# Optimization experiments

Measured on AMD Instinct MI355X. Metric: run time of the kernel, lower is better.

Reference implementation:

```python
import math
import jax, jax.numpy as jnp
import numpy as np

B, T = 4, 512
STATE_DIM, ACT_DIM = 17, 18
H, NH, L, MAXT = 1024, 16, 4, 4096
S = 3 * T          # interleaved (rtg, state, action) sequence length
D = H // NH
FF = 4 * H
LN_EPS = 1e-5


def setup_inputs() -> dict:
    key = jax.random.key(0)
    ks = jax.random.split(key, 32)
    init = lambda k, shape: jax.random.normal(k, shape, jnp.float32) * 0.02
    inp = {
        "states": jax.random.normal(ks[0], (B, T, STATE_DIM), jnp.float32),
        "returns_to_go": jax.random.normal(ks[1], (B, T, 1), jnp.float32),
        "timesteps": jax.random.randint(ks[2], (B, T), 0, MAXT),
        "actions": jax.random.randint(ks[3], (B, T), 0, ACT_DIM),
        "bandera": 0,
        # embeddings / input projections
        "embed_time_table": init(ks[4], (MAXT, H)),
        "embed_act_table": init(ks[5], (ACT_DIM, H)),
        "Wrtg": init(ks[6], (1, H)), "brtg": jnp.zeros((H,), jnp.float32),
        "Wst": init(ks[7], (STATE_DIM, H)), "bst": jnp.zeros((H,), jnp.float32),
        # per-block params, stacked over L layers
        "Wq": init(ks[8], (L, H, H)), "bq": jnp.zeros((L, H), jnp.float32),
        "Wk": init(ks[9], (L, H, H)), "bk": jnp.zeros((L, H), jnp.float32),
        "Wv": init(ks[10], (L, H, H)), "bv": jnp.zeros((L, H), jnp.float32),
        "Wo": init(ks[11], (L, H, H)), "bo": jnp.zeros((L, H), jnp.float32),
        "W1": init(ks[12], (L, H, FF)), "b1": jnp.zeros((L, FF), jnp.float32),
        "W2": init(ks[13], (L, FF, H)), "b2": jnp.zeros((L, H), jnp.float32),
        # prediction heads
        "Wpr": init(ks[14], (H, 1)), "bpr": jnp.zeros((1,), jnp.float32),
        "Wps": init(ks[15], (H, STATE_DIM)), "bps": jnp.zeros((STATE_DIM,), jnp.float32),
        "Wpa": init(ks[16], (H, ACT_DIM)), "bpa": jnp.zeros((ACT_DIM,), jnp.float32),
    }
    return inp


def _ln(x):
    # LayerNorm, elementwise_affine=False
    m = jnp.mean(x, axis=-1, keepdims=True)
    v = jnp.mean((x - m) ** 2, axis=-1, keepdims=True)
    return (x - m) * jax.lax.rsqrt(v + LN_EPS)


def reference(states, returns_to_go, embed_time_table, embed_act_table,
              Wrtg, brtg, Wst, bst,
              Wq, bq, Wk, bk, Wv, bv, Wo, bo,
              W1, b1, W2, b2,
              Wpr, bpr, Wps, bps, Wpa, bpa,
              timesteps, actions, bandera):
    te = embed_time_table[timesteps]                      # [B,T,H]
    r = returns_to_go @ Wrtg + brtg + te                  # [B,T,H]
    s = states @ Wst + bst + te                           # [B,T,H]
    a = embed_act_table[actions] + te                     # [B,T,H]
    # interleave (r_t, s_t, a_t) along time -> [B, 3T, H]
    h = jnp.stack([r, s, a], axis=2).reshape(B, S, H)
    h = _ln(h)
    mask = jnp.tril(jnp.ones((S, S), bool))
    scale = 1.0 / math.sqrt(D)
    for i in range(L):
        q = (h @ Wq[i] + bq[i]).reshape(B, S, NH, D).transpose(0, 2, 1, 3)
        k = (h @ Wk[i] + bk[i]).reshape(B, S, NH, D).transpose(0, 2, 1, 3)
        v = (h @ Wv[i] + bv[i]).reshape(B, S, NH, D).transpose(0, 2, 1, 3)
        sc = jnp.einsum('bhqd,bhkd->bhqk', q, k) * scale  # [B,NH,S,S]
        sc = jnp.where(mask, sc, -jnp.inf)
        att = jax.nn.softmax(sc, axis=-1)
        o = jnp.einsum('bhqk,bhkd->bhqd', att, v)
        o = o.transpose(0, 2, 1, 3).reshape(B, S, H)
        h = _ln(h + o @ Wo[i] + bo[i])
        m = jax.nn.gelu(h @ W1[i] + b1[i], approximate=False) @ W2[i] + b2[i]
        h = _ln(h + m)
    hh = h.reshape(B, T, 3, H)
    h_s = hh[:, :, 1]   # token after (..., r_t, s_t)
    h_a = hh[:, :, 2]   # token after (..., r_t, s_t, a_t)
    return_preds = h_a @ Wpr + bpr                        # [B,T,1]
    state_preds = h_a @ Wps + bps                         # [B,T,STATE_DIM]
    action_preds = h_s @ Wpa + bpa                        # [B,T,ACT_DIM]
    return (state_preds, action_preds, return_preds)
```

## Files before the change

### kernel.cpp

```cpp
#include <hip/hip_runtime.h>
#include <hip/hip_bf16.h>
#include <math.h>

#define Bc 4
#define Tc 512
#define Sc 1536
#define Hc 1024
#define NHc 16
#define Dc 64
#define FFc 4096
#define Lc 4
#define Mrows (Bc*Tc*3)
#define LN_EPS 1e-5f

typedef __attribute__((ext_vector_type(4))) float  f32x4;
typedef __attribute__((ext_vector_type(8))) short  s16x8;
typedef __attribute__((ext_vector_type(4))) short  s16x4;

__device__ __forceinline__ short f2b(float f) {
    union { __hip_bfloat16 h; short s; } u;
    u.h = __float2bfloat16(f);
    return u.s;
}

__device__ __forceinline__ void gload16(const void* g, void* l) {
    __builtin_amdgcn_global_load_lds(
        (const __attribute__((address_space(1))) void*)g,
        (__attribute__((address_space(3))) void*)l, 16, 0, 0);
}

__global__ __launch_bounds__(256) void embed_kernel(
    const float* __restrict__ states, const float* __restrict__ rtg,
    const int* __restrict__ timesteps, const int* __restrict__ actions,
    const float* __restrict__ ett, const float* __restrict__ eat,
    const float* __restrict__ Wrtg, const float* __restrict__ brtg,
    const float* __restrict__ Wst, const float* __restrict__ bst,
    float* __restrict__ h)
{
    const int bt = blockIdx.x;
    const int b = bt / Tc, t = bt % Tc;
    const int ts = timesteps[bt];
    const int ac = actions[bt];
    const float rv = rtg[bt];
    const float* te = ett + (size_t)ts * Hc;
    const float* ea = eat + (size_t)ac * Hc;
    __shared__ float sst[17];
    if (threadIdx.x < 17) sst[threadIdx.x] = states[bt * 17 + threadIdx.x];
    __syncthreads();
    float* hr = h + ((size_t)b * Sc + 3 * t) * Hc;
    for (int j = threadIdx.x; j < Hc; j += 256) {
        const float tej = te[j];
        hr[j] = rv * Wrtg[j] + brtg[j] + tej;
        float sv = bst[j];
        #pragma unroll
        for (int qx = 0; qx < 17; ++qx) sv += sst[qx] * Wst[qx * Hc + j];
        hr[Hc + j] = sv + tej;
        hr[2 * Hc + j] = ea[j] + tej;
    }
}

__global__ __launch_bounds__(256) void resln_kernel(float* __restrict__ h,
                                                    const float* __restrict__ add,
                                                    short* __restrict__ hb)
{
    const size_t row = blockIdx.x;
    float4* hr = reinterpret_cast<float4*>(h + row * Hc);
    const int tid = threadIdx.x;
    float4 x = hr[tid];
    if (add != nullptr) {
        const float4 a = reinterpret_cast<const float4*>(add + row * Hc)[tid];
        x.x += a.x; x.y += a.y; x.z += a.z; x.w += a.w;
    }
    float s1 = x.x + x.y + x.z + x.w;
    float s2 = x.x*x.x + x.y*x.y + x.z*x.z + x.w*x.w;
    #pragma unroll
    for (int off = 32; off > 0; off >>= 1) {
        s1 += __shfl_xor(s1, off);
        s2 += __shfl_xor(s2, off);
    }
    __shared__ float r1[4], r2[4];
    const int wv = tid >> 6, lane = tid & 63;
    if (lane == 0) { r1[wv] = s1; r2[wv] = s2; }
    __syncthreads();
    s1 = r1[0] + r1[1] + r1[2] + r1[3];
    s2 = r2[0] + r2[1] + r2[2] + r2[3];
    const float mean = s1 * (1.0f / Hc);
    const float var  = s2 * (1.0f / Hc) - mean * mean;
    const float rs = rsqrtf(var + LN_EPS);
    x.x = (x.x - mean) * rs; x.y = (x.y - mean) * rs;
    x.z = (x.z - mean) * rs; x.w = (x.w - mean) * rs;
    hr[tid] = x;
    if (hb != nullptr) {
        s16x4 o; o[0] = f2b(x.x); o[1] = f2b(x.y); o[2] = f2b(x.z); o[3] = f2b(x.w);
        *(s16x4*)&hb[row * Hc + tid * 4] = o;
    }
}

__global__ __launch_bounds__(256) void wconv_all_kernel(
    const float* __restrict__ Wq, const float* __restrict__ Wk,
    const float* __restrict__ Wv, const float* __restrict__ Wo,
    const float* __restrict__ W1, const float* __restrict__ W2,
    short* __restrict__ wqkv_t, short* __restrict__ wo_t,
    short* __restrict__ w1_t, short* __restrict__ w2_t)
{
    __shared__ float Ls[64][68];
    const int blk = blockIdx.x;
    const float* src; short* dst; int N, dstStride, dstRow0, tx, ty;
    if (blk < 1024) {
        const int m = blk >> 8;
        const int local = blk & 255;
        tx = local & 15; ty = local >> 4;
        N = 1024; dstStride = 1024;
        if (m == 0)      { src = Wq; dst = wqkv_t; dstRow0 = 0; }
        else if (m == 1) { src = Wk; dst = wqkv_t; dstRow0 = 1024; }
        else if (m == 2) { src = Wv; dst = wqkv_t; dstRow0 = 2048; }
        else             { src = Wo; dst = wo_t;   dstRow0 = 0; }
    } else if (blk < 2048) {
        const int local = blk - 1024;
        tx = local & 63; ty = local >> 6;
        src = W1; dst = w1_t; N = 4096; dstStride = 1024; dstRow0 = 0;
    } else {
        const int local = blk - 2048;
        tx = local & 15; ty = local >> 4;
        src = W2; dst = w2_t; N = 1024; dstStride = 4096; dstRow0 = 0;
    }
    const int n0 = tx * 64, k0 = ty * 64;
    const int tid = threadIdx.x;
    #pragma unroll
    for (int it = 0; it < 4; ++it) {
        const int idx = tid + 256 * it;
        const int r = idx >> 4, c4 = idx & 15;
        *(f32x4*)&Ls[r][c4 * 4] = *(const f32x4*)(src + (size_t)(k0 + r) * N + n0 + c4 * 4);
    }
    __syncthreads();
    #pragma unroll
    for (int it = 0; it < 2; ++it) {
        const int idx = tid + 256 * it;
        const int n = idx & 63, k8 = idx >> 6;
        s16x8 o;
        #pragma unroll
        for (int j = 0; j < 8; ++j) o[j] = f2b(Ls[k8 * 8 + j][n]);
        *(s16x8*)(dst + (size_t)(dstRow0 + n0 + n) * dstStride + k0 + k8 * 8) = o;
    }
}

__global__ __launch_bounds__(256) void biaspack_kernel(
    const float* __restrict__ bq, const float* __restrict__ bk,
    const float* __restrict__ bv, float* __restrict__ pb)
{
    const int idx = blockIdx.x * 256 + threadIdx.x;
    const int l = idx / 3072, j = idx % 3072;
    float v;
    if (j < 1024) v = bq[l * 1024 + j];
    else if (j < 2048) v = bk[l * 1024 + j - 1024];
    else v = bv[l * 1024 + j - 2048];
    pb[idx] = v;
}

__global__ __launch_bounds__(256) void headspack_kernel(
    const float* __restrict__ Wps, const float* __restrict__ bps,
    const float* __restrict__ Wpr, const float* __restrict__ bpr,
    const float* __restrict__ Wpa, const float* __restrict__ bpa,
    short* __restrict__ Wha, short* __restrict__ Whb,
    float* __restrict__ biasA, float* __restrict__ biasB)
{
    const int n = blockIdx.x & 63, set = blockIdx.x >> 6;
    const int tid = threadIdx.x;
    if (tid == 0) {
        if (set == 0) biasA[n] = (n < 17) ? bps[n] : (n == 17 ? bpr[0] : 0.f);
        else          biasB[n] = (n < 18) ? bpa[n] : 0.f;
    }
    short* dst = (set == 0 ? Wha : Whb) + (size_t)n * 1024;
    for (int k = tid; k < 1024; k += 256) {
        float v;
        if (set == 0) v = (n < 17) ? Wps[(size_t)k * 17 + n] : (n == 17 ? Wpr[k] : 0.f);
        else          v = (n < 18) ? Wpa[(size_t)k * 18 + n] : 0.f;
        dst[k] = f2b(v);
    }
}

__global__ __launch_bounds__(256) void headsgather_kernel(
    const float* __restrict__ scrA, const float* __restrict__ scrB,
    float* __restrict__ out)
{
    const int idx = blockIdx.x * 256 + threadIdx.x;
    if (idx >= 2048 * 36) return;
    const int bt = idx / 36, j = idx % 36;
    if (j < 17)      out[bt * 17 + j] = scrA[bt * 64 + j];
    else if (j < 35) out[2048 * 17 + bt * 18 + (j - 17)] = scrB[bt * 64 + (j - 17)];
    else             out[2048 * 35 + bt] = scrA[bt * 64 + 17];
}

template<int BN, int DO_GELU, int OUTBF16>
__global__ __launch_bounds__(256) void gemm_bb(
    const short* __restrict__ A, const short* __restrict__ Bt,
    const float* __restrict__ bias, void* __restrict__ Cv,
    int M, int N, int K, int arm, int aro)
{
    constexpr int NJ = BN / 32;
    __shared__ short As[2 * 128 * 32];
    __shared__ short Bs[2 * BN * 32];
    const int tid = threadIdx.x, lane = tid & 63, wid = tid >> 6;
    const int wr = wid >> 1, wc = wid & 1;
    const int g = lane >> 4, ql = lane & 15;
    const int m0 = blockIdx.y * 128, n0 = blockIdx.x * BN;

    const int crow = lane >> 2;
    const int ccol = (lane & 3) * 8;

    const short* Ag0 = A + ((size_t)arm * (m0 + wid * 32 + crow) + aro) * K + ccol;
    const short* Ag1 = A + ((size_t)arm * (m0 + wid * 32 + 16 + crow) + aro) * K + ccol;
    const int a0off = (wid * 32) * 32;
    const int a1off = (wid * 32 + 16) * 32;

    const short* Bg0; const short* Bg1 = nullptr;
    int b0off = 0, b1off = 0;
    if constexpr (BN == 128) {
        Bg0 = Bt + (size_t)(n0 + wid * 32 + crow) * K + ccol;
        Bg1 = Bt + (size_t)(n0 + wid * 32 + 16 + crow) * K + ccol;
        b0off = (wid * 32) * 32;
        b1off = (wid * 32 + 16) * 32;
    } else {
        Bg0 = Bt + (size_t)(n0 + wid * 16 + crow) * K + ccol;
        b0off = (wid * 16) * 32;
    }

    auto stage = [&](int buf, int k0) {
        short* Ab = &As[buf * (128 * 32)];
        short* Bb = &Bs[buf * (BN * 32)];
        gload16(Ag0 + k0, Ab + a0off);
        gload16(Ag1 + k0, Ab + a1off);
        gload16(Bg0 + k0, Bb + b0off);
        if constexpr (BN == 128) gload16(Bg1 + k0, Bb + b1off);
    };

    f32x4 acc[4][NJ] = {};
    stage(0, 0);
    int cur = 0;
    for (int k0 = 0; k0 < K; k0 += 32) {
        __syncthreads();
        if (k0 + 32 < K) stage(cur ^ 1, k0 + 32);
        const short* Acur = &As[cur * (128 * 32)];
        const short* Bcur = &Bs[cur * (BN * 32)];
        s16x8 af[4], bfr[NJ];
        #pragma unroll
        for (int mi = 0; mi < 4; ++mi)
            af[mi] = *(const s16x8*)&Acur[(wr * 64 + mi * 16 + ql) * 32 + g * 8];
        #pragma unroll
        for (int nj = 0; nj < NJ; ++nj)
            bfr[nj] = *(const s16x8*)&Bcur[(wc * (BN / 2) + nj * 16 + ql) * 32 + g * 8];
        #pragma unroll
        for (int mi = 0; mi < 4; ++mi)
            #pragma unroll
            for (int nj = 0; nj < NJ; ++nj)
                acc[mi][nj] = __builtin_amdgcn_mfma_f32_16x16x32_bf16(
                    af[mi], bfr[nj], acc[mi][nj], 0, 0, 0);
        cur ^= 1;
    }

    #pragma unroll
    for (int mi = 0; mi < 4; ++mi) {
        #pragma unroll
        for (int nj = 0; nj < NJ; ++nj) {
            const int col = n0 + wc * (BN / 2) + nj * 16 + ql;
            const float bv = bias[col];
            #pragma unroll
            for (int r = 0; r < 4; ++r) {
                const int row = m0 + wr * 64 + mi * 16 + g * 4 + r;
                float v = acc[mi][nj][r] + bv;
                if constexpr (DO_GELU)
                    v = 0.5f * v * (1.0f + erff(v * 0.70710678118654752f));
                if constexpr (OUTBF16)
                    ((short*)Cv)[(size_t)row * N + col] = f2b(v);
                else
                    ((float*)Cv)[(size_t)row * N + col] = v;
            }
        }
    }
}

template<int BN, int ABF16, int DO_GELU, int OUTBF16>
__global__ __launch_bounds__(256) void gemm_mfma(
    const void* __restrict__ Av, const float* __restrict__ Wg,
    const float* __restrict__ bias, void* __restrict__ Cv,
    int M, int N, int K, int ldw)
{
    constexpr int NJ = BN / 32;
    __shared__ short As[128][32];
    __shared__ short Bs[BN][40];
    const int tid  = threadIdx.x;
    const int lane = tid & 63;
    const int wid  = tid >> 6;
    const int wr   = wid >> 1, wc = wid & 1;
    const int m0 = blockIdx.y * 128;
    const int n0 = blockIdx.x * BN;

    const int  wn4  = tid >> 3;
    const int  wk4  = (tid & 7) * 4;
    const bool wact = tid < 2 * BN;

    f32x4 areg[4]; s16x8 abreg[2]; f32x4 wreg[4];

    auto loadA = [&](int k0) {
        if constexpr (!ABF16) {
            const float* A = (const float*)Av;
            #pragma unroll
            for (int i = 0; i < 4; ++i) {
                const int idx = tid + 256 * i;
                const int r = idx >> 3, c4 = idx & 7;
                areg[i] = *(const f32x4*)(A + (size_t)(m0 + r) * K + k0 + c4 * 4);
            }
        } else {
            const short* A = (const short*)Av;
            #pragma unroll
            for (int i = 0; i < 2; ++i) {
                const int idx = tid + 256 * i;
                const int r = idx >> 2, c = idx & 3;
                abreg[i] = *(const s16x8*)(A + (size_t)(m0 + r) * K + k0 + c * 8);
            }
        }
    };
    auto loadW = [&](int k0) {
        if (wact) {
            #pragma unroll
            for (int i = 0; i < 4; ++i)
                wreg[i] = *(const f32x4*)(Wg + (size_t)(k0 + wk4 + i) * ldw + n0 + wn4 * 4);
        }
    };
    auto stage = [&]() {
        if constexpr (!ABF16) {
            #pragma unroll
            for (int i = 0; i < 4; ++i) {
                const int idx = tid + 256 * i;
                const int r = idx >> 3, c4 = idx & 7;
                s16x4 s;
                #pragma unroll
                for (int j = 0; j < 4; ++j) s[j] = f2b(areg[i][j]);
                *(s16x4*)&As[r][c4 * 4] = s;
            }
        } else {
            #pragma unroll
            for (int i = 0; i < 2; ++i) {
                const int idx = tid + 256 * i;
                const int r = idx >> 2, c = idx & 3;
                *(s16x8*)&As[r][c * 8] = abreg[i];
            }
        }
        if (wact) {
            #pragma unroll
            for (int j = 0; j < 4; ++j) {
                s16x4 o;
                #pragma unroll
                for (int i = 0; i < 4; ++i) o[i] = f2b(wreg[i][j]);
                *(s16x4*)&Bs[wn4 * 4 + j][wk4] = o;
            }
        }
    };

    f32x4 acc[4][NJ] = {};

    loadA(0); loadW(0);
    for (int k0 = 0; k0 < K; k0 += 32) {
        __syncthreads();
        stage();
        __syncthreads();
        if (k0 + 32 < K) { loadA(k0 + 32); loadW(k0 + 32); }
        s16x8 af[4], bfr[NJ];
        #pragma unroll
        for (int mi = 0; mi < 4; ++mi)
            af[mi] = *(const s16x8*)&As[wr * 64 + mi * 16 + (lane & 15)][(lane >> 4) * 8];
        #pragma unroll
        for (int nj = 0; nj < NJ; ++nj)
            bfr[nj] = *(const s16x8*)&Bs[wc * (BN / 2) + nj * 16 + (lane & 15)][(lane >> 4) * 8];
        #pragma unroll
        for (int mi = 0; mi < 4; ++mi)
            #pragma unroll
            for (int nj = 0; nj < NJ; ++nj)
                acc[mi][nj] = __builtin_amdgcn_mfma_f32_16x16x32_bf16(
                    af[mi], bfr[nj], acc[mi][nj], 0, 0, 0);
    }

    #pragma unroll
    for (int mi = 0; mi < 4; ++mi) {
        #pragma unroll
        for (int nj = 0; nj < NJ; ++nj) {
            const int col = n0 + wc * (BN / 2) + nj * 16 + (lane & 15);
            const float bv = bias[col];
            #pragma unroll
            for (int r = 0; r < 4; ++r) {
                const int row = m0 + wr * 64 + mi * 16 + (lane >> 4) * 4 + r;
                float v = acc[mi][nj][r] + bv;
                if constexpr (DO_GELU)
                    v = 0.5f * v * (1.0f + erff(v * 0.70710678118654752f));
                if constexpr (OUTBF16)
                    ((short*)Cv)[(size_t)row * N + col] = f2b(v);
                else
                    ((float*)Cv)[(size_t)row * N + col] = v;
            }
        }
    }
}

__global__ __launch_bounds__(256) void vtrans_kernel(
    const short* __restrict__ v, int vs, short* __restrict__ vt)
{
    const int nkt = Sc / 64;
    const int blk = blockIdx.x;
    const int bh = blk / nkt, kt = blk % nkt;
    const int b = bh / NHc, hh = bh % NHc;
    __shared__ short Ls[64][64];
    const int tid = threadIdx.x;
    #pragma unroll
    for (int i = 0; i < 2; ++i) {
        const int idx = tid + 256 * i;
        const int r = idx >> 3, c8 = idx & 7;
        const int cs = c8 ^ (r & 7) ^ (r >> 3);
        *(s16x8*)&Ls[r][cs * 8] =
            *(const s16x8*)(v + ((size_t)(b * Sc + kt * 64 + r)) * vs + hh * 64 + c8 * 8);
    }
    __syncthreads();
    #pragma unroll
    for (int i = 0; i < 2; ++i) {
        const int idx = tid + 256 * i;
        const int d = idx >> 3, k8 = idx & 7;
        s16x8 o;
        #pragma unroll
        for (int j = 0; j < 8; ++j) {
            const int kv = k8 * 8 + j;
            const int cs = (d >> 3) ^ (kv & 7) ^ (kv >> 3);
            o[j] = Ls[kv][cs * 8 + (d & 7)];
        }
        *(s16x8*)(vt + ((size_t)bh * 64 + d) * Sc + kt * 64 + k8 * 8) = o;
    }
}

__global__ __launch_bounds__(256) void attn_kernel(
    const short* __restrict__ qg, const short* __restrict__ kg,
    const short* __restrict__ vtg, short* __restrict__ og, int qks)
{
    const int nqt = Sc / 64;
    const int blk = blockIdx.x;
    const int bh = blk / nqt;
    const int qt = (nqt - 1) - (blk % nqt);
    const int b = bh / NHc, hh = bh % NHc;
    const int tid = threadIdx.x, lane = tid & 63, w = tid >> 6;
    const int g = lane >> 4, ql = lane & 15;

    __shared__ short Qs[64][72];
    __shared__ short Ks[64][72];
    __shared__ short Vs[64][72];
    __shared__ short Ps[4][16][72];

    const size_t baseq = ((size_t)b * Sc) * qks + hh * Dc;

    #pragma unroll
    for (int i = 0; i < 2; ++i) {
        const int idx = tid + 256 * i;
        const int r = idx >> 3, c8 = idx & 7;
        *(s16x8*)&Qs[r][c8 * 8] =
            *(const s16x8*)(qg + baseq + (size_t)(qt * 64 + r) * qks + c8 * 8);
    }
    __syncthreads();
    const s16x8 bq0 = *(const s16x8*)&Qs[w * 16 + ql][g * 8];
    const s16x8 bq1 = *(const s16x8*)&Qs[w * 16 + ql][32 + g * 8];

    f32x4 acc_o[4] = {};
    float m = -1e30f, l = 0.f;
    const int qrow = qt * 64 + w * 16 + ql;

    for (int kt = 0; kt <= qt; ++kt) {
        __syncthreads();
        #pragma unroll
        for (int i = 0; i < 2; ++i) {
            const int idx = tid + 256 * i;
            const int r = idx >> 3, c8 = idx & 7;
            *(s16x8*)&Ks[r][c8 * 8] =
                *(const s16x8*)(kg + baseq + (size_t)(kt * 64 + r) * qks + c8 * 8);
            *(s16x8*)&Vs[r][c8 * 8] =
                *(const s16x8*)(vtg + ((size_t)bh * 64 + r) * Sc + kt * 64 + c8 * 8);
        }
        __syncthreads();

        f32x4 sacc[4] = {};
        #pragma unroll
        for (int mi = 0; mi < 4; ++mi) {
            const s16x8 a0 = *(const s16x8*)&Ks[mi * 16 + ql][g * 8];
            const s16x8 a1 = *(const s16x8*)&Ks[mi * 16 + ql][32 + g * 8];
            sacc[mi] = __builtin_amdgcn_mfma_f32_16x16x32_bf16(a0, bq0, sacc[mi], 0, 0, 0);
            sacc[mi] = __builtin_amdgcn_mfma_f32_16x16x32_bf16(a1, bq1, sacc[mi], 0, 0, 0);
        }

        float pv[16];
        float pm = -1e30f;
        #pragma unroll
        for (int mi = 0; mi < 4; ++mi)
            #pragma unroll
            for (int r = 0; r < 4; ++r) {
                const int kv = kt * 64 + mi * 16 + g * 4 + r;
                const float s = (kv <= qrow) ? sacc[mi][r] * 0.125f : -1e30f;
                pv[mi * 4 + r] = s;
                pm = fmaxf(pm, s);
            }
        pm = fmaxf(pm, __shfl_xor(pm, 16));
        pm = fmaxf(pm, __shfl_xor(pm, 32));
        const float m2 = fmaxf(m, pm);
        const float corr = __expf(m - m2);
        m = m2;
        float ps = 0.f;
        #pragma unroll
        for (int i = 0; i < 16; ++i) { pv[i] = __expf(pv[i] - m2); ps += pv[i]; }
        ps += __shfl_xor(ps, 16);
        ps += __shfl_xor(ps, 32);
        l = l * corr + ps;

        #pragma unroll
        for (int mi = 0; mi < 4; ++mi) {
            s16x4 pw;
            #pragma unroll
            for (int r = 0; r < 4; ++r) pw[r] = f2b(pv[mi * 4 + r]);
            *(s16x4*)&Ps[w][ql][mi * 16 + g * 4] = pw;
        }

        float corr_r[4];
        #pragma unroll
        for (int r = 0; r < 4; ++r) corr_r[r] = __shfl(corr, g * 4 + r);
        #pragma unroll
        for (int nj = 0; nj < 4; ++nj)
            #pragma unroll
            for (int r = 0; r < 4; ++r) acc_o[nj][r] *= corr_r[r];

        const s16x8 pa0 = *(const s16x8*)&Ps[w][ql][g * 8];
        const s16x8 pa1 = *(const s16x8*)&Ps[w][ql][32 + g * 8];
        #pragma unroll
        for (int nj = 0; nj < 4; ++nj) {
            const s16x8 v0 = *(const s16x8*)&Vs[nj * 16 + ql][g * 8];
            const s16x8 v1 = *(const s16x8*)&Vs[nj * 16 + ql][32 + g * 8];
            acc_o[nj] = __builtin_amdgcn_mfma_f32_16x16x32_bf16(pa0, v0, acc_o[nj], 0, 0, 0);
            acc_o[nj] = __builtin_amdgcn_mfma_f32_16x16x32_bf16(pa1, v1, acc_o[nj], 0, 0, 0);
        }
    }

    const float rl = 1.0f / l;
    float rl_r[4];
    #pragma unroll
    for (int r = 0; r < 4; ++r) rl_r[r] = __shfl(rl, g * 4 + r);
    const size_t baseo = ((size_t)b * Sc) * Hc + hh * Dc;
    #pragma unroll
    for (int nj = 0; nj < 4; ++nj)
        #pragma unroll
        for (int r = 0; r < 4; ++r) {
            const int qr = qt * 64 + w * 16 + g * 4 + r;
            og[baseo + (size_t)qr * Hc + nj * 16 + ql] = f2b(acc_o[nj][r] * rl_r[r]);
        }
}

__global__ __launch_bounds__(64) void heads_kernel(
    const float* __restrict__ h,
    const float* __restrict__ Wpr, const float* __restrict__ bpr,
    const float* __restrict__ Wps, const float* __restrict__ bps,
    const float* __restrict__ Wpa, const float* __restrict__ bpa,
    float* __restrict__ out)
{
    const int bt = blockIdx.x;
    const int b = bt / Tc, t = bt % Tc;
    const float* hs = h + ((size_t)b * Sc + 3 * t + 1) * Hc;
    const float* ha = h + ((size_t)b * Sc + 3 * t + 2) * Hc;
    __shared__ float shs[Hc], sha[Hc];
    for (int i = threadIdx.x; i < Hc; i += 64) { shs[i] = hs[i]; sha[i] = ha[i]; }
    __syncthreads();
    const int j = threadIdx.x;
    if (j < 17) {
        float a = bps[j];
        for (int kx = 0; kx < Hc; ++kx) a += sha[kx] * Wps[kx * 17 + j];
        out[bt * 17 + j] = a;
    } else if (j < 35) {
        const int jj = j - 17;
        float a = bpa[jj];
        for (int kx = 0; kx < Hc; ++kx) a += shs[kx] * Wpa[kx * 18 + jj];
        out[Bc * Tc * 17 + bt * 18 + jj] = a;
    } else if (j == 35) {
        float a = bpr[0];
        for (int kx = 0; kx < Hc; ++kx) a += sha[kx] * Wpr[kx];
        out[Bc * Tc * 35 + bt] = a;
    }
}

extern "C" void kernel_launch(void* const* d_in, const int* in_sizes, int n_in,
                              void* d_out, int out_size, void* d_ws, size_t ws_size,
                              hipStream_t stream)
{
    const float* states = (const float*)d_in[0];
    const float* rtg    = (const float*)d_in[1];
    const int*   timesteps = (const int*)d_in[2];
    const int*   actions   = (const int*)d_in[3];
    const float* ett  = (const float*)d_in[5];
    const float* eat  = (const float*)d_in[6];
    const float* Wrtg = (const float*)d_in[7];
    const float* brtg = (const float*)d_in[8];
    const float* Wst  = (const float*)d_in[9];
    const float* bst  = (const float*)d_in[10];
    const float* Wq = (const float*)d_in[11];
    const float* bq = (const float*)d_in[12];
    const float* Wk = (const float*)d_in[13];
    const float* bk = (const float*)d_in[14];
    const float* Wv = (const float*)d_in[15];
    const float* bv = (const float*)d_in[16];
    const float* Wo = (const float*)d_in[17];
    const float* bo = (const float*)d_in[18];
    const float* W1 = (const float*)d_in[19];
    const float* b1 = (const float*)d_in[20];
    const float* W2 = (const float*)d_in[21];
    const float* b2 = (const float*)d_in[22];
    const float* Wpr = (const float*)d_in[23];
    const float* bpr = (const float*)d_in[24];
    const float* Wps = (const float*)d_in[25];
    const float* bps = (const float*)d_in[26];
    const float* Wpa = (const float*)d_in[27];
    const float* bpa = (const float*)d_in[28];
    float* out = (float*)d_out;

    char* wsb = (char*)d_ws;
    const size_t MH = (size_t)Mrows * Hc;
    const int nAttnBlk = Bc * NHc * (Sc / 64);

    const size_t off_h    = 0;
    const size_t off_hb   = off_h    + MH * 4;
    const size_t off_qkv  = off_hb   + MH * 2;
    const size_t off_vt   = off_qkv  + MH * 6;
    const size_t off_ob   = off_vt   + MH * 2;
    const size_t off_rb   = off_ob   + MH * 2;
    const size_t off_wl   = off_rb   + MH * 4;
    const size_t wl_qkv   = 0;
    const size_t wl_wo    = wl_qkv + (size_t)3072 * 1024 * 2;
    const size_t wl_w1    = wl_wo  + (size_t)1024 * 1024 * 2;
    const size_t wl_w2    = wl_w1  + (size_t)4096 * 1024 * 2;
    const size_t wl_bytes = wl_w2  + (size_t)1024 * 4096 * 2;
    const size_t off_pb   = off_wl + wl_bytes;
    const size_t NEED     = off_pb + (size_t)Lc * 3072 * 4;

    if (ws_size >= NEED) {
        float* h   = (float*)(wsb + off_h);
        short* hb  = (short*)(wsb + off_hb);
        short* qkv = (short*)(wsb + off_qkv);
        short* vt  = (short*)(wsb + off_vt);
        short* ob  = (short*)(wsb + off_ob);
        float* rb  = (float*)(wsb + off_rb);
        short* gb  = qkv;
        short* wqkv_t = (short*)(wsb + off_wl + wl_qkv);
        short* wo_t   = (short*)(wsb + off_wl + wl_wo);
        short* w1_t   = (short*)(wsb + off_wl + wl_w1);
        short* w2_t   = (short*)(wsb + off_wl + wl_w2);
        float* pb     = (float*)(wsb + off_pb);
        short* Wha   = vt;
        short* Whb   = vt + 64 * 1024;
        float* biasA = (float*)(vt + 2 * 64 * 1024);
        float* biasB = biasA + 64;
        float* scrA  = rb;
        float* scrB  = rb + 2048 * 64;

        biaspack_kernel<<<Lc * 12, 256, 0, stream>>>(bq, bk, bv, pb);
        embed_kernel<<<Bc * Tc, 256, 0, stream>>>(states, rtg, timesteps, actions,
                                                  ett, eat, Wrtg, brtg, Wst, bst, h);
        resln_kernel<<<Mrows, 256, 0, stream>>>(h, nullptr, hb);

        const dim3 gQKV(3072 / 128, Mrows / 128);
        const dim3 gFF1(FFc / 128, Mrows / 128);
        const dim3 gN1K(1024 / 128, Mrows / 128);

        for (int i = 0; i < Lc; ++i) {
            const size_t wofH = (size_t)i * Hc * Hc;
            const size_t wofF = (size_t)i * Hc * FFc;
            wconv_all_kernel<<<3072, 256, 0, stream>>>(
                Wq + wofH, Wk + wofH, Wv + wofH, Wo + wofH, W1 + wofF, W2 + wofF,
                wqkv_t, wo_t, w1_t, w2_t);

            gemm_bb<128,0,1><<<gQKV, 256, 0, stream>>>(hb, wqkv_t, pb + i * 3072, qkv, Mrows, 3072, 1024, 1, 0);
            vtrans_kernel<<<nAttnBlk, 256, 0, stream>>>(qkv + 2048, 3072, vt);
            attn_kernel<<<nAttnBlk, 256, 0, stream>>>(qkv, qkv + 1024, vt, ob, 3072);
            gemm_bb<128,0,0><<<gN1K, 256, 0, stream>>>(ob, wo_t, bo + i * Hc, rb, Mrows, 1024, 1024, 1, 0);
            resln_kernel<<<Mrows, 256, 0, stream>>>(h, rb, hb);

            gemm_bb<128,1,1><<<gFF1, 256, 0, stream>>>(hb, w1_t, b1 + i * FFc, gb, Mrows, 4096, 1024, 1, 0);
            gemm_bb<128,0,0><<<gN1K, 256, 0, stream>>>(gb, w2_t, b2 + i * Hc, rb, Mrows, 1024, 4096, 1, 0);
            resln_kernel<<<Mrows, 256, 0, stream>>>(h, rb, hb);
        }

        headspack_kernel<<<128, 256, 0, stream>>>(Wps, bps, Wpr, bpr, Wpa, bpa,
                                                  Wha, Whb, biasA, biasB);
        gemm_bb<64,0,0><<<dim3(1, 16), 256, 0, stream>>>(hb, Wha, biasA, scrA, 2048, 64, 1024, 3, 2);
        gemm_bb<64,0,0><<<dim3(1, 16), 256, 0, stream>>>(hb, Whb, biasB, scrB, 2048, 64, 1024, 3, 1);
        headsgather_kernel<<<288, 256, 0, stream>>>(scrA, scrB, out);
    } else {
        float* h  = (float*)wsb;
        short* qb = (short*)(wsb + MH * 4);
        short* kb = (short*)(wsb + MH * 6);
        short* vb = (short*)(wsb + MH * 8);
        short* vt = (short*)(wsb + MH * 10);
        float* rb = (float*)(wsb + MH * 12);
        short* gb = qb;

        const dim3 g64(Hc / 64, Mrows / 128);
        const dim3 g128(FFc / 128, Mrows / 128);

        embed_kernel<<<Bc * Tc, 256, 0, stream>>>(states, rtg, timesteps, actions,
                                                  ett, eat, Wrtg, brtg, Wst, bst, h);
        resln_kernel<<<Mrows, 256, 0, stream>>>(h, nullptr, nullptr);

        for (int i = 0; i < Lc; ++i) {
            const size_t wof = (size_t)i * Hc * Hc;
            gemm_mfma<64,0,0,1><<<g64, 256, 0, stream>>>(h, Wq + wof, bq + i * Hc, qb, Mrows, Hc, Hc, Hc);
            gemm_mfma<64,0,0,1><<<g64, 256, 0, stream>>>(h, Wk + wof, bk + i * Hc, kb, Mrows, Hc, Hc, Hc);
            gemm_mfma<64,0,0,1><<<g64, 256, 0, stream>>>(h, Wv + wof, bv + i * Hc, vb, Mrows, Hc, Hc, Hc);
            vtrans_kernel<<<nAttnBlk, 256, 0, stream>>>(vb, 1024, vt);
            attn_kernel<<<nAttnBlk, 256, 0, stream>>>(qb, kb, vt, qb, 1024);
            gemm_mfma<64,1,0,0><<<g64, 256, 0, stream>>>(qb, Wo + wof, bo + i * Hc, rb, Mrows, Hc, Hc, Hc);
            resln_kernel<<<Mrows, 256, 0, stream>>>(h, rb, nullptr);

            const float* W1i = W1 + (size_t)i * Hc * FFc;
            const float* b1i = b1 + (size_t)i * FFc;
            const float* W2i = W2 + (size_t)i * FFc * Hc;
            gemm_mfma<128,0,1,1><<<g128, 256, 0, stream>>>(h, W1i, b1i, gb, Mrows, FFc, Hc, FFc);
            gemm_mfma<64,1,0,0><<<g64, 256, 0, stream>>>(gb, W2i, b2 + i * Hc, rb, Mrows, Hc, FFc, Hc);
            resln_kernel<<<Mrows, 256, 0, stream>>>(h, rb, nullptr);
        }

        heads_kernel<<<Bc * Tc, 64, 0, stream>>>(h, Wpr, bpr, Wps, bps, Wpa, bpa, out);
    }
}
```

Baseline: 1.664 ms.

## Swizzle GEMM LDS layout and prefetch two K-tiles ahead with explicit waitcnt

The bf16 GEMM's global-to-LDS loads and fragment reads now use an XOR swizzle on the 8-element column slot, so wave-level LDS reads avoid bank conflicts. The main loop is restructured to prefetch two stages ahead. Explicit vmcnt waits replace the blanket __syncthreads, and a second barrier after fragment reads lets the next tile's loads be issued into the just-consumed buffer before the MFMAs run. This is meant to hide global load latency and cut LDS conflicts. It relies on exact knowledge of how many outstanding vector-memory ops gload16 issues, which is fragile.

```diff
diff --git a/kernel.cpp b/kernel.cpp
--- a/kernel.cpp
+++ b/kernel.cpp
@@ -206,22 +206,22 @@
     const int m0 = blockIdx.y * 128, n0 = blockIdx.x * BN;
 
     const int crow = lane >> 2;
-    const int ccol = (lane & 3) * 8;
-
-    const short* Ag0 = A + ((size_t)arm * (m0 + wid * 32 + crow) + aro) * K + ccol;
-    const short* Ag1 = A + ((size_t)arm * (m0 + wid * 32 + 16 + crow) + aro) * K + ccol;
+    const int csw  = ((lane & 3) ^ ((crow >> 1) & 3)) * 8;
+
+    const short* Ag0 = A + ((size_t)arm * (m0 + wid * 32 + crow) + aro) * K + csw;
+    const short* Ag1 = A + ((size_t)arm * (m0 + wid * 32 + 16 + crow) + aro) * K + csw;
     const int a0off = (wid * 32) * 32;
     const int a1off = (wid * 32 + 16) * 32;
 
     const short* Bg0; const short* Bg1 = nullptr;
     int b0off = 0, b1off = 0;
     if constexpr (BN == 128) {
-        Bg0 = Bt + (size_t)(n0 + wid * 32 + crow) * K + ccol;
-        Bg1 = Bt + (size_t)(n0 + wid * 32 + 16 + crow) * K + ccol;
+        Bg0 = Bt + (size_t)(n0 + wid * 32 + crow) * K + csw;
+        Bg1 = Bt + (size_t)(n0 + wid * 32 + 16 + crow) * K + csw;
         b0off = (wid * 32) * 32;
         b1off = (wid * 32 + 16) * 32;
     } else {
-        Bg0 = Bt + (size_t)(n0 + wid * 16 + crow) * K + ccol;
+        Bg0 = Bt + (size_t)(n0 + wid * 16 + crow) * K + csw;
         b0off = (wid * 16) * 32;
     }
 
@@ -234,21 +234,39 @@
         if constexpr (BN == 128) gload16(Bg1 + k0, Bb + b1off);
     };
 
+    const int rslot = (g ^ ((ql >> 1) & 3)) * 8;
+    const int aoffr = (wr * 64 + ql) * 32 + rslot;
+    const int boffr = (wc * (BN / 2) + ql) * 32 + rslot;
+
     f32x4 acc[4][NJ] = {};
     stage(0, 0);
+    stage(1, 32);
     int cur = 0;
     for (int k0 = 0; k0 < K; k0 += 32) {
-        __syncthreads();
-        if (k0 + 32 < K) stage(cur ^ 1, k0 + 32);
+        if (k0 + 32 < K) {
+            if constexpr (BN == 128) asm volatile("s_waitcnt vmcnt(4)" ::: "memory");
+            else                     asm volatile("s_waitcnt vmcnt(3)" ::: "memory");
+        } else {
+            asm volatile("s_waitcnt vmcnt(0)" ::: "memory");
+        }
+        __builtin_amdgcn_s_barrier();
+
         const short* Acur = &As[cur * (128 * 32)];
         const short* Bcur = &Bs[cur * (BN * 32)];
         s16x8 af[4], bfr[NJ];
         #pragma unroll
         for (int mi = 0; mi < 4; ++mi)
-            af[mi] = *(const s16x8*)&Acur[(wr * 64 + mi * 16 + ql) * 32 + g * 8];
+            af[mi] = *(const s16x8*)&Acur[aoffr + mi * (16 * 32)];
         #pragma unroll
         for (int nj = 0; nj < NJ; ++nj)
-            bfr[nj] = *(const s16x8*)&Bcur[(wc * (BN / 2) + nj * 16 + ql) * 32 + g * 8];
+            bfr[nj] = *(const s16x8*)&Bcur[boffr + nj * (16 * 32)];
+
+        asm volatile("s_waitcnt lgkmcnt(0)" ::: "memory");
+        __builtin_amdgcn_sched_barrier(0);
+        __builtin_amdgcn_s_barrier();
+
+        if (k0 + 64 < K) stage(cur, k0 + 64);
+
         #pragma unroll
         for (int mi = 0; mi < 4; ++mi)
             #pragma unroll
```

Measured after the change: 1.578 ms. -5.1%, faster.
